# Kernel optimization log

Measured on AMD Instinct MI355X. Metric: run time of the kernel, lower is better.

Reference implementation:

```python
import jax, jax.numpy as jnp
import numpy as np

D_MODEL = 512
N_HEADS = 8
D_K = D_MODEL // N_HEADS


def setup_inputs() -> dict:
    key = jax.random.key(0)
    ks = jax.random.split(key, 11)
    B, L, D = 2, 4096, D_MODEL
    s = 1.0 / np.sqrt(D)
    return {
        "q": jax.random.normal(ks[0], (B, L, D), jnp.float32),
        "k": jax.random.normal(ks[1], (B, L, D), jnp.float32),
        "v": jax.random.normal(ks[2], (B, L, D), jnp.float32),
        "Wq": jax.random.normal(ks[3], (D, D), jnp.float32) * s,
        "bq": jnp.zeros((D,), jnp.float32),
        "Wk": jax.random.normal(ks[4], (D, D), jnp.float32) * s,
        "bk": jnp.zeros((D,), jnp.float32),
        "Wv": jax.random.normal(ks[5], (D, D), jnp.float32) * s,
        "bv": jnp.zeros((D,), jnp.float32),
        "Wo": jax.random.normal(ks[6], (D, D), jnp.float32) * s,
        "bo": jnp.zeros((D,), jnp.float32),
    }


def reference(q, k, v, Wq, bq, Wk, bk, Wv, bv, Wo, bo):
    B, L, D = q.shape
    H, dk = N_HEADS, D_K
    # projections -> [B, H, L, dk]
    qh = (q @ Wq + bq).reshape(B, L, H, dk).transpose(0, 2, 1, 3)
    kh = (k @ Wk + bk).reshape(B, -1, H, dk).transpose(0, 2, 1, 3)
    vh = (v @ Wv + bv).reshape(B, -1, H, dk).transpose(0, 2, 1, 3)
    scores = jnp.einsum("bhqd,bhkd->bhqk", qh, kh) / jnp.sqrt(jnp.float32(dk))
    attn = jax.nn.softmax(scores, axis=-1)  # dropout: eval-mode identity
    ctx = jnp.einsum("bhqk,bhkd->bhqd", attn, vh)
    ctx = ctx.transpose(0, 2, 1, 3).reshape(B, L, D)
    return ctx @ Wo + bo
```

## Files before the change

kernel.cpp:

```cpp
#include <hip/hip_runtime.h>
#include <hip/hip_bf16.h>

#define NB 2
#define NL 4096
#define ND 512
#define NH 8
#define NDK 64
#define NM (NB * NL)
#define QSCALE 0.18033688011112042f

typedef short bf16x8_t __attribute__((ext_vector_type(8)));
typedef float f32x4_t __attribute__((ext_vector_type(4)));

static __device__ __forceinline__ unsigned short f2bs(float f) {
  union { float f; unsigned u; } c; c.f = f;
  unsigned r = c.u + 0x7fffu + ((c.u >> 16) & 1u);
  return (unsigned short)(r >> 16);
}
static __device__ __forceinline__ float bs2f(unsigned short s) {
  union { unsigned u; float f; } c; c.u = ((unsigned)s) << 16; return c.f;
}
static __device__ __forceinline__ unsigned pk_bf16(float a, float b) {
  union { __hip_bfloat162 h; unsigned u; } c;
  c.h = __float22bfloat162_rn(make_float2(a, b));
  return c.u;
}

__global__ __launch_bounds__(256)
void round3_kernel(const float* __restrict__ s0, const float* __restrict__ s1,
                   const float* __restrict__ s2, unsigned short* __restrict__ d0,
                   unsigned short* __restrict__ d1, unsigned short* __restrict__ d2)
{
  const float* s = blockIdx.y == 0 ? s0 : (blockIdx.y == 1 ? s1 : s2);
  unsigned short* d = blockIdx.y == 0 ? d0 : (blockIdx.y == 1 ? d1 : d2);
  const size_t i = ((size_t)blockIdx.x * 256 + threadIdx.x) * 8;
  const float4 f0 = *(const float4*)(s + i);
  const float4 f1 = *(const float4*)(s + i + 4);
  uint4 o;
  o.x = pk_bf16(f0.x, f0.y);
  o.y = pk_bf16(f0.z, f0.w);
  o.z = pk_bf16(f1.x, f1.y);
  o.w = pk_bf16(f1.z, f1.w);
  *(uint4*)(d + i) = o;
}

struct WArgs {
  const float* W[4];
  unsigned short* Th[4];
  unsigned short* Tl[4];
};
__global__ __launch_bounds__(256)
void wsplit_kernel(WArgs a)
{
  const int z = blockIdx.z;
  const float* __restrict__ W = a.W[z];
  const int tid = threadIdx.x;
  const int n = blockIdx.x * 64 + (tid & 63);
  const int kb = blockIdx.y * 64 + (tid >> 6) * 16;
  unsigned short h[16], l[16];
#pragma unroll
  for (int u = 0; u < 16; ++u) {
    const float x = W[(size_t)(kb + u) * ND + n];
    h[u] = f2bs(x);
    l[u] = f2bs(x - bs2f(h[u]));
  }
  unsigned wh[8], wl[8];
#pragma unroll
  for (int p = 0; p < 8; ++p) {
    wh[p] = (unsigned)h[2 * p] | ((unsigned)h[2 * p + 1] << 16);
    wl[p] = (unsigned)l[2 * p] | ((unsigned)l[2 * p + 1] << 16);
  }
  unsigned short* th = a.Th[z] + (size_t)n * ND + kb;
  unsigned short* tl = a.Tl[z] + (size_t)n * ND + kb;
  *(uint4*)th = make_uint4(wh[0], wh[1], wh[2], wh[3]);
  *(uint4*)(th + 8) = make_uint4(wh[4], wh[5], wh[6], wh[7]);
  *(uint4*)tl = make_uint4(wl[0], wl[1], wl[2], wl[3]);
  *(uint4*)(tl + 8) = make_uint4(wl[4], wl[5], wl[6], wl[7]);
}

template <bool ASPLIT, int NJ, int OUTMODE>
__device__ __forceinline__ void gemm_core(
    const unsigned short* __restrict__ Ahi, const unsigned short* __restrict__ Alo,
    const unsigned short* __restrict__ Bh, const unsigned short* __restrict__ Bl,
    const float* __restrict__ bias, unsigned short* __restrict__ outH,
    float* __restrict__ outF, int m0, int n0, float scale)
{
  __shared__ unsigned short AH[128][36];
  __shared__ unsigned short AL[ASPLIT ? 128 : 1][36];
  __shared__ unsigned short BHs[NJ * 16][36];
  __shared__ unsigned short BLs[NJ * 16][36];

  const int tid = threadIdx.x;
  const int lane = tid & 63, w = tid >> 6;
  const int m = lane & 15, quad = lane >> 4;
  const int r = tid >> 1, hf = (tid & 1) * 16;
  const int rb = (NJ == 8) ? (tid >> 1) : (tid >> 2);
  const int cb = (NJ == 8) ? ((tid & 1) * 16) : ((tid & 3) * 8);

  const unsigned short* aRow = Ahi + (size_t)(m0 + r) * ND + hf;
  const unsigned short* alRow = ASPLIT ? (Alo + (size_t)(m0 + r) * ND + hf) : nullptr;
  const unsigned short* bhRow = Bh + (size_t)(n0 + rb) * ND + cb;
  const unsigned short* blRow = Bl + (size_t)(n0 + rb) * ND + cb;

  uint4 ra0 = *(const uint4*)(aRow);
  uint4 ra1 = *(const uint4*)(aRow + 8);
  uint4 rl0, rl1;
  if constexpr (ASPLIT) {
    rl0 = *(const uint4*)(alRow);
    rl1 = *(const uint4*)(alRow + 8);
  }
  uint4 rbh0 = *(const uint4*)(bhRow);
  uint4 rbl0 = *(const uint4*)(blRow);
  uint4 rbh1, rbl1;
  if constexpr (NJ == 8) {
    rbh1 = *(const uint4*)(bhRow + 8);
    rbl1 = *(const uint4*)(blRow + 8);
  }

  f32x4_t acc[2][NJ];
#pragma unroll
  for (int i = 0; i < 2; ++i)
#pragma unroll
    for (int j = 0; j < NJ; ++j) acc[i][j] = (f32x4_t){0.f, 0.f, 0.f, 0.f};

  for (int k0 = 0; k0 < ND; k0 += 32) {
    __syncthreads();
    *(uint4*)&AH[r][hf] = ra0;
    *(uint4*)&AH[r][hf + 8] = ra1;
    if constexpr (ASPLIT) {
      *(uint4*)&AL[r][hf] = rl0;
      *(uint4*)&AL[r][hf + 8] = rl1;
    }
    *(uint4*)&BHs[rb][cb] = rbh0;
    *(uint4*)&BLs[rb][cb] = rbl0;
    if constexpr (NJ == 8) {
      *(uint4*)&BHs[rb][cb + 8] = rbh1;
      *(uint4*)&BLs[rb][cb + 8] = rbl1;
    }
    if (k0 + 32 < ND) {
      const int kn = k0 + 32;
      ra0 = *(const uint4*)(aRow + kn);
      ra1 = *(const uint4*)(aRow + kn + 8);
      if constexpr (ASPLIT) {
        rl0 = *(const uint4*)(alRow + kn);
        rl1 = *(const uint4*)(alRow + kn + 8);
      }
      rbh0 = *(const uint4*)(bhRow + kn);
      rbl0 = *(const uint4*)(blRow + kn);
      if constexpr (NJ == 8) {
        rbh1 = *(const uint4*)(bhRow + kn + 8);
        rbl1 = *(const uint4*)(blRow + kn + 8);
      }
    }
    __syncthreads();

    bf16x8_t ah[2], al[2];
#pragma unroll
    for (int i = 0; i < 2; ++i) {
      ah[i] = *(const bf16x8_t*)&AH[w * 32 + 16 * i + m][quad * 8];
      if constexpr (ASPLIT) al[i] = *(const bf16x8_t*)&AL[w * 32 + 16 * i + m][quad * 8];
    }
#pragma unroll
    for (int j = 0; j < NJ; ++j) {
      const bf16x8_t bhj = *(const bf16x8_t*)&BHs[16 * j + m][quad * 8];
      const bf16x8_t blj = *(const bf16x8_t*)&BLs[16 * j + m][quad * 8];
#pragma unroll
      for (int i = 0; i < 2; ++i) {
        acc[i][j] = __builtin_amdgcn_mfma_f32_16x16x32_bf16(ah[i], bhj, acc[i][j], 0, 0, 0);
        acc[i][j] = __builtin_amdgcn_mfma_f32_16x16x32_bf16(ah[i], blj, acc[i][j], 0, 0, 0);
        if constexpr (ASPLIT)
          acc[i][j] = __builtin_amdgcn_mfma_f32_16x16x32_bf16(al[i], bhj, acc[i][j], 0, 0, 0);
      }
    }
  }

  if constexpr (OUTMODE != 2) {
#pragma unroll
    for (int i = 0; i < 2; ++i)
#pragma unroll
      for (int rr = 0; rr < 4; ++rr) {
        const int mg = m0 + w * 32 + 16 * i + quad * 4 + rr;
#pragma unroll
        for (int j = 0; j < NJ; ++j) {
          const int n = n0 + 16 * j + m;
          const float c = (acc[i][j][rr] + bias[n]) * scale;
          if constexpr (OUTMODE == 0) {
            const int b = mg >> 12, l = mg & (NL - 1);
            const int h = n >> 6, d = n & (NDK - 1);
            outH[(((size_t)(b * NH + h)) * NL + l) * NDK + d] = f2bs(c);
          } else {
            outF[(size_t)mg * ND + n] = c;
          }
        }
      }
  } else {
    unsigned short* T = &BHs[0][0];
    const int bb = m0 >> 12;
    const int lbase = m0 & (NL - 1);
#pragma unroll 1
    for (int p = 0; p < 4; ++p) {
      __syncthreads();
      if (w == p) {
#pragma unroll
        for (int i = 0; i < 2; ++i)
#pragma unroll
          for (int j = 0; j < NJ; ++j) {
            const int n = 16 * j + m;
            const float bv = bias[n0 + n];
            const unsigned w0 = pk_bf16((acc[i][j][0] + bv) * scale,
                                        (acc[i][j][1] + bv) * scale);
            const unsigned w1 = pk_bf16((acc[i][j][2] + bv) * scale,
                                        (acc[i][j][3] + bv) * scale);
            *(uint2*)&T[n * 34 + 16 * i + quad * 4] = make_uint2(w0, w1);
          }
      }
      __syncthreads();
      const int n = tid >> 1;
      const int l0 = (tid & 1) * 16;
      const uint4 t0 = *(const uint4*)&T[n * 34 + l0];
      const uint4 t1 = *(const uint4*)&T[n * 34 + l0 + 8];
      const int ng = n0 + n;
      const int h = ng >> 6, d = ng & (NDK - 1);
      unsigned short* dp =
          outH + (((size_t)(bb * NH + h)) * NDK + d) * NL + lbase + 32 * p + l0;
      *(uint4*)dp = t0;
      *(uint4*)(dp + 8) = t1;
    }
  }
}

struct ProjArgs {
  const unsigned short* A[3];
  const unsigned short* Bh[3];
  const unsigned short* Bl[3];
  const float* bias[3];
  unsigned short* out[3];
  float scale[3];
};
__global__ __launch_bounds__(256, 3)
void gemm_proj_kernel(ProjArgs a)
{
  const int z = blockIdx.z;
  if (z < 2)
    gemm_core<false, 8, 0>(a.A[z], nullptr, a.Bh[z], a.Bl[z], a.bias[z], a.out[z],
                           nullptr, blockIdx.x * 128, blockIdx.y * 128, a.scale[z]);
  else
    gemm_core<false, 8, 2>(a.A[2], nullptr, a.Bh[2], a.Bl[2], a.bias[2], a.out[2],
                           nullptr, blockIdx.x * 128, blockIdx.y * 128, a.scale[2]);
}
__global__ __launch_bounds__(256, 3)
void gemm_out_kernel(const unsigned short* __restrict__ Ahi,
                     const unsigned short* __restrict__ Alo,
                     const unsigned short* __restrict__ Bh,
                     const unsigned short* __restrict__ Bl,
                     const float* __restrict__ bias, float* __restrict__ out)
{
  gemm_core<true, 4, 1>(Ahi, Alo, Bh, Bl, bias, nullptr, out,
                        blockIdx.x * 128, blockIdx.y * 64, 1.0f);
}

__global__ __launch_bounds__(256, 4)
void attn_kernel(const unsigned short* __restrict__ qh, const unsigned short* __restrict__ kh,
                 const unsigned short* __restrict__ vt_g, float* __restrict__ op,
                 float* __restrict__ lp)
{
  __shared__ unsigned short Ks[64][72];
  __shared__ unsigned short Vt[64][72];
  __shared__ unsigned Pt[64][67];

  const int tid = threadIdx.x;
  const int w = tid >> 6;
  const int lane = tid & 63;
  const int m = lane & 15;
  const int quad = lane >> 4;

  const int bid = blockIdx.x;
  const int half = bid & 1;
  const int qt = (bid >> 1) & 31;
  const int bh = bid >> 6;
  const int kt0 = half * 32, kt1 = kt0 + 32;
  const unsigned short* qb = qh + (size_t)bh * NL * NDK;
  const unsigned short* kb = kh + (size_t)bh * NL * NDK;
  const unsigned short* vb = vt_g + (size_t)bh * NDK * NL;

  bf16x8_t aq[2][2];
#pragma unroll
  for (int mt = 0; mt < 2; ++mt) {
    const unsigned short* qsrc =
        qb + (size_t)(qt * 128 + w * 32 + mt * 16 + m) * NDK + quad * 8;
    aq[mt][0] = *(const bf16x8_t*)(qsrc);
    aq[mt][1] = *(const bf16x8_t*)(qsrc + 32);
  }

  const short ob = (short)0x3F80;
  const bf16x8_t ones = {ob, ob, ob, ob, ob, ob, ob, ob};

  f32x4_t o[2][4];
#pragma unroll
  for (int mt = 0; mt < 2; ++mt)
#pragma unroll
    for (int nt = 0; nt < 4; ++nt) o[mt][nt] = (f32x4_t){0.f, 0.f, 0.f, 0.f};
  f32x4_t ol[2];
  ol[0] = (f32x4_t){0.f, 0.f, 0.f, 0.f};
  ol[1] = (f32x4_t){0.f, 0.f, 0.f, 0.f};

  const int kr = tid >> 2;
  const int kc = (tid & 3) * 16;

  uint4 pk0, pk1, pv0, pv1;
  {
    const unsigned short* ksrc = kb + (size_t)(kt0 * 64 + kr) * NDK + kc;
    pk0 = *(const uint4*)ksrc;
    pk1 = *(const uint4*)(ksrc + 8);
    const unsigned short* vsrc = vb + (size_t)kr * NL + kt0 * 64 + kc;
    pv0 = *(const uint4*)vsrc;
    pv1 = *(const uint4*)(vsrc + 8);
  }

  for (int kt = kt0; kt < kt1; ++kt) {
    __syncthreads();
    *(uint4*)&Ks[kr][kc] = pk0;
    *(uint4*)&Ks[kr][kc + 8] = pk1;
    *(uint4*)&Vt[kr][kc] = pv0;
    *(uint4*)&Vt[kr][kc + 8] = pv1;
    if (kt + 1 < kt1) {
      const unsigned short* ksrc = kb + (size_t)((kt + 1) * 64 + kr) * NDK + kc;
      pk0 = *(const uint4*)ksrc;
      pk1 = *(const uint4*)(ksrc + 8);
      const unsigned short* vsrc = vb + (size_t)kr * NL + (kt + 1) * 64 + kc;
      pv0 = *(const uint4*)vsrc;
      pv1 = *(const uint4*)(vsrc + 8);
    }
    __syncthreads();

#pragma unroll
    for (int nt = 0; nt < 4; ++nt) {
      const bf16x8_t b0 = *(const bf16x8_t*)&Ks[16 * nt + m][quad * 8];
      const bf16x8_t b1 = *(const bf16x8_t*)&Ks[16 * nt + m][quad * 8 + 32];
      f32x4_t s0 = (f32x4_t){0.f, 0.f, 0.f, 0.f};
      s0 = __builtin_amdgcn_mfma_f32_16x16x32_bf16(aq[0][0], b0, s0, 0, 0, 0);
      s0 = __builtin_amdgcn_mfma_f32_16x16x32_bf16(aq[0][1], b1, s0, 0, 0, 0);
      f32x4_t s1 = (f32x4_t){0.f, 0.f, 0.f, 0.f};
      s1 = __builtin_amdgcn_mfma_f32_16x16x32_bf16(aq[1][0], b0, s1, 0, 0, 0);
      s1 = __builtin_amdgcn_mfma_f32_16x16x32_bf16(aq[1][1], b1, s1, 0, 0, 0);
      unsigned pw[4];
#pragma unroll
      for (int r = 0; r < 4; ++r)
        pw[r] = pk_bf16(exp2f(s0[r]), exp2f(s1[r]));
      *(uint4*)&Pt[16 * nt + m][w * 16 + quad * 4] =
          make_uint4(pw[0], pw[1], pw[2], pw[3]);
    }

#pragma unroll
    for (int kb2 = 0; kb2 < 2; ++kb2) {
      unsigned pwv[8];
#pragma unroll
      for (int j = 0; j < 8; ++j)
        pwv[j] = Pt[kb2 * 32 + quad * 8 + j][w * 16 + m];
      union { bf16x8_t v; unsigned d[4]; } pa0, pa1;
#pragma unroll
      for (int t = 0; t < 4; ++t) {
        pa0.d[t] = (pwv[2 * t] & 0xffffu) | (pwv[2 * t + 1] << 16);
        pa1.d[t] = (pwv[2 * t] >> 16) | (pwv[2 * t + 1] & 0xffff0000u);
      }
#pragma unroll
      for (int nt = 0; nt < 4; ++nt) {
        const bf16x8_t vb0 = *(const bf16x8_t*)&Vt[16 * nt + m][kb2 * 32 + quad * 8];
        o[0][nt] = __builtin_amdgcn_mfma_f32_16x16x32_bf16(pa0.v, vb0, o[0][nt], 0, 0, 0);
        o[1][nt] = __builtin_amdgcn_mfma_f32_16x16x32_bf16(pa1.v, vb0, o[1][nt], 0, 0, 0);
      }
      ol[0] = __builtin_amdgcn_mfma_f32_16x16x32_bf16(pa0.v, ones, ol[0], 0, 0, 0);
      ol[1] = __builtin_amdgcn_mfma_f32_16x16x32_bf16(pa1.v, ones, ol[1], 0, 0, 0);
    }
  }

  const size_t pbase = (size_t)(half * 16 + bh) * NL;
#pragma unroll
  for (int mt = 0; mt < 2; ++mt) {
    const int q0 = qt * 128 + w * 32 + mt * 16 + quad * 4;
    if (m == 0)
      *(float4*)&lp[pbase + q0] =
          make_float4(ol[mt][0], ol[mt][1], ol[mt][2], ol[mt][3]);
#pragma unroll
    for (int r = 0; r < 4; ++r) {
      float* dst = op + (pbase + q0 + r) * NDK;
#pragma unroll
      for (int nt = 0; nt < 4; ++nt) dst[16 * nt + m] = o[mt][nt][r];
    }
  }
}

__global__ __launch_bounds__(256)
void merge_kernel(const float* __restrict__ op, const float* __restrict__ lp,
                  unsigned short* __restrict__ ctxh, unsigned short* __restrict__ ctxl)
{
  const size_t t = (size_t)blockIdx.x * 256 + threadIdx.x;
  const int d0 = (int)(t & 7) * 8;
  const size_t row = t >> 3;
  const float l0 = lp[row];
  const float l1 = lp[row + (size_t)16 * NL];
  const float inv = 1.0f / (l0 + l1);
  const float* a = op + row * NDK + d0;
  const float* c = a + (size_t)16 * NL * NDK;
  const float4 a0 = *(const float4*)a, a1 = *(const float4*)(a + 4);
  const float4 c0 = *(const float4*)c, c1 = *(const float4*)(c + 4);
  const float x[8] = {(a0.x + c0.x) * inv, (a0.y + c0.y) * inv,
                      (a0.z + c0.z) * inv, (a0.w + c0.w) * inv,
                      (a1.x + c1.x) * inv, (a1.y + c1.y) * inv,
                      (a1.z + c1.z) * inv, (a1.w + c1.w) * inv};
  unsigned short hs[8], ls[8];
#pragma unroll
  for (int u = 0; u < 8; ++u) {
    hs[u] = f2bs(x[u]);
    ls[u] = f2bs(x[u] - bs2f(hs[u]));
  }
  const int bh = (int)(row >> 12), l = (int)(row & (NL - 1));
  const int b = bh >> 3, h = bh & 7;
  const size_t dst = ((size_t)(b * NL + l)) * ND + h * 64 + d0;
  uint4 uh, ul;
  uh.x = (unsigned)hs[0] | ((unsigned)hs[1] << 16);
  uh.y = (unsigned)hs[2] | ((unsigned)hs[3] << 16);
  uh.z = (unsigned)hs[4] | ((unsigned)hs[5] << 16);
  uh.w = (unsigned)hs[6] | ((unsigned)hs[7] << 16);
  ul.x = (unsigned)ls[0] | ((unsigned)ls[1] << 16);
  ul.y = (unsigned)ls[2] | ((unsigned)ls[3] << 16);
  ul.z = (unsigned)ls[4] | ((unsigned)ls[5] << 16);
  ul.w = (unsigned)ls[6] | ((unsigned)ls[7] << 16);
  *(uint4*)(ctxh + dst) = uh;
  *(uint4*)(ctxl + dst) = ul;
}

extern "C" void kernel_launch(void* const* d_in, const int* in_sizes, int n_in,
                              void* d_out, int out_size, void* d_ws, size_t ws_size,
                              hipStream_t stream)
{
  const float* q  = (const float*)d_in[0];
  const float* k  = (const float*)d_in[1];
  const float* v  = (const float*)d_in[2];
  const float* Wq = (const float*)d_in[3];
  const float* bq = (const float*)d_in[4];
  const float* Wk = (const float*)d_in[5];
  const float* bk = (const float*)d_in[6];
  const float* Wv = (const float*)d_in[7];
  const float* bv = (const float*)d_in[8];
  const float* Wo = (const float*)d_in[9];
  const float* bo = (const float*)d_in[10];

  const size_t PLANE = (size_t)NM * ND;
  unsigned short* wt = (unsigned short*)d_ws;
  unsigned short* qhp = wt + 8 * (size_t)ND * ND;
  unsigned short* khp = qhp + PLANE;
  unsigned short* vtp = khp + PLANE;
  float* op = (float*)(vtp + PLANE);
  float* lp = op + 2 * (size_t)16 * NL * NDK;
  unsigned short* qb = (unsigned short*)op;
  unsigned short* kb = qb + PLANE;
  unsigned short* vb = kb + PLANE;
  unsigned short* ctxh = qhp;
  unsigned short* ctxl = khp;

  unsigned short* wth[4], *wtl[4];
  for (int i = 0; i < 4; ++i) {
    wth[i] = wt + (size_t)(2 * i) * ND * ND;
    wtl[i] = wt + (size_t)(2 * i + 1) * ND * ND;
  }

  round3_kernel<<<dim3(PLANE / (256 * 8), 3), 256, 0, stream>>>(q, k, v, qb, kb, vb);

  WArgs wa;
  wa.W[0] = Wq; wa.W[1] = Wk; wa.W[2] = Wv; wa.W[3] = Wo;
  for (int i = 0; i < 4; ++i) { wa.Th[i] = wth[i]; wa.Tl[i] = wtl[i]; }
  wsplit_kernel<<<dim3(8, 8, 4), 256, 0, stream>>>(wa);

  ProjArgs pa;
  pa.A[0] = qb; pa.A[1] = kb; pa.A[2] = vb;
  pa.Bh[0] = wth[0]; pa.Bl[0] = wtl[0];
  pa.Bh[1] = wth[1]; pa.Bl[1] = wtl[1];
  pa.Bh[2] = wth[2]; pa.Bl[2] = wtl[2];
  pa.bias[0] = bq; pa.bias[1] = bk; pa.bias[2] = bv;
  pa.out[0] = qhp; pa.out[1] = khp; pa.out[2] = vtp;
  pa.scale[0] = QSCALE; pa.scale[1] = 1.0f; pa.scale[2] = 1.0f;
  gemm_proj_kernel<<<dim3(NM / 128, ND / 128, 3), 256, 0, stream>>>(pa);

  attn_kernel<<<dim3(NB * NH * (NL / 128) * 2), 256, 0, stream>>>(qhp, khp, vtp, op, lp);

  merge_kernel<<<dim3((16 * NL * NDK) / (256 * 8)), 256, 0, stream>>>(op, lp, ctxh, ctxl);

  gemm_out_kernel<<<dim3(NM / 128, ND / 64), 256, 0, stream>>>(
      ctxh, ctxl, wth[3], wtl[3], bo, (float*)d_out);
}
```

Baseline: 289.4 us.

## Keep P in registers via transposed QK^T, swizzle LDS, enlarge query tile

Computes S^T = K·Q^T so the MFMA output layout lines up directly with the A-operand layout for the P·V product, so the Pt shared-memory round trip and its repacking are gone. K and V tiles are stored in LDS with an XOR swizzle instead of padding. Each wave now handles 64 query rows (256 per block), which doubles reuse of every K/V tile loaded and halves the grid. In exchange, register pressure rises (launch bounds drop to 2 blocks per CU) and there are fewer blocks in flight.

```diff
diff --git a/kernel.cpp b/kernel.cpp
--- a/kernel.cpp
+++ b/kernel.cpp
@@ -259,35 +259,35 @@
                         blockIdx.x * 128, blockIdx.y * 64, 1.0f);
 }
 
-__global__ __launch_bounds__(256, 4)
+__global__ __launch_bounds__(256, 2)
 void attn_kernel(const unsigned short* __restrict__ qh, const unsigned short* __restrict__ kh,
                  const unsigned short* __restrict__ vt_g, float* __restrict__ op,
                  float* __restrict__ lp)
 {
-  __shared__ unsigned short Ks[64][72];
-  __shared__ unsigned short Vt[64][72];
-  __shared__ unsigned Pt[64][67];
+  __shared__ unsigned short Ks[64 * 64];
+  __shared__ unsigned short Vt[64 * 64];
 
   const int tid = threadIdx.x;
   const int w = tid >> 6;
   const int lane = tid & 63;
   const int m = lane & 15;
   const int quad = lane >> 4;
+  const int sw = m & 7;
 
   const int bid = blockIdx.x;
   const int half = bid & 1;
-  const int qt = (bid >> 1) & 31;
-  const int bh = bid >> 6;
+  const int qt = (bid >> 1) & 15;
+  const int bh = bid >> 5;
   const int kt0 = half * 32, kt1 = kt0 + 32;
   const unsigned short* qb = qh + (size_t)bh * NL * NDK;
   const unsigned short* kb = kh + (size_t)bh * NL * NDK;
   const unsigned short* vb = vt_g + (size_t)bh * NDK * NL;
 
-  bf16x8_t aq[2][2];
-#pragma unroll
-  for (int mt = 0; mt < 2; ++mt) {
+  bf16x8_t aq[4][2];
+#pragma unroll
+  for (int mt = 0; mt < 4; ++mt) {
     const unsigned short* qsrc =
-        qb + (size_t)(qt * 128 + w * 32 + mt * 16 + m) * NDK + quad * 8;
+        qb + (size_t)(qt * 256 + w * 64 + mt * 16 + m) * NDK + quad * 8;
     aq[mt][0] = *(const bf16x8_t*)(qsrc);
     aq[mt][1] = *(const bf16x8_t*)(qsrc + 32);
   }
@@ -295,17 +295,26 @@
   const short ob = (short)0x3F80;
   const bf16x8_t ones = {ob, ob, ob, ob, ob, ob, ob, ob};
 
-  f32x4_t o[2][4];
-#pragma unroll
-  for (int mt = 0; mt < 2; ++mt)
+  f32x4_t o[4][4];
+#pragma unroll
+  for (int mt = 0; mt < 4; ++mt)
 #pragma unroll
     for (int nt = 0; nt < 4; ++nt) o[mt][nt] = (f32x4_t){0.f, 0.f, 0.f, 0.f};
-  f32x4_t ol[2];
-  ol[0] = (f32x4_t){0.f, 0.f, 0.f, 0.f};
-  ol[1] = (f32x4_t){0.f, 0.f, 0.f, 0.f};
+  f32x4_t ol[4];
+#pragma unroll
+  for (int mt = 0; mt < 4; ++mt) ol[mt] = (f32x4_t){0.f, 0.f, 0.f, 0.f};
 
   const int kr = tid >> 2;
-  const int kc = (tid & 3) * 16;
+  const int kcb = tid & 3;
+  const int kc = kcb * 16;
+  const int r7 = kr & 7;
+  const int st0 = kr * 64 + ((2 * kcb) ^ r7) * 8;
+  const int st1 = kr * 64 + ((2 * kcb + 1) ^ r7) * 8;
+
+  const int rowb = m * 64;
+  const int ck0 = rowb + ((quad ^ sw) * 8);
+  const int ck1 = rowb + (((quad + 4) ^ sw) * 8);
+  const int vq = quad >> 1, vo = (quad & 1) * 4;
 
   uint4 pk0, pk1, pv0, pv1;
   {
@@ -319,10 +328,10 @@
 
   for (int kt = kt0; kt < kt1; ++kt) {
     __syncthreads();
-    *(uint4*)&Ks[kr][kc] = pk0;
-    *(uint4*)&Ks[kr][kc + 8] = pk1;
-    *(uint4*)&Vt[kr][kc] = pv0;
-    *(uint4*)&Vt[kr][kc + 8] = pv1;
+    *(uint4*)&Ks[st0] = pk0;
+    *(uint4*)&Ks[st1] = pk1;
+    *(uint4*)&Vt[st0] = pv0;
+    *(uint4*)&Vt[st1] = pv1;
     if (kt + 1 < kt1) {
       const unsigned short* ksrc = kb + (size_t)((kt + 1) * 64 + kr) * NDK + kc;
       pk0 = *(const uint4*)ksrc;
@@ -334,50 +343,51 @@
     __syncthreads();
 
 #pragma unroll
-    for (int nt = 0; nt < 4; ++nt) {
-      const bf16x8_t b0 = *(const bf16x8_t*)&Ks[16 * nt + m][quad * 8];
-      const bf16x8_t b1 = *(const bf16x8_t*)&Ks[16 * nt + m][quad * 8 + 32];
-      f32x4_t s0 = (f32x4_t){0.f, 0.f, 0.f, 0.f};
-      s0 = __builtin_amdgcn_mfma_f32_16x16x32_bf16(aq[0][0], b0, s0, 0, 0, 0);
-      s0 = __builtin_amdgcn_mfma_f32_16x16x32_bf16(aq[0][1], b1, s0, 0, 0, 0);
-      f32x4_t s1 = (f32x4_t){0.f, 0.f, 0.f, 0.f};
-      s1 = __builtin_amdgcn_mfma_f32_16x16x32_bf16(aq[1][0], b0, s1, 0, 0, 0);
-      s1 = __builtin_amdgcn_mfma_f32_16x16x32_bf16(aq[1][1], b1, s1, 0, 0, 0);
-      unsigned pw[4];
-#pragma unroll
-      for (int r = 0; r < 4; ++r)
-        pw[r] = pk_bf16(exp2f(s0[r]), exp2f(s1[r]));
-      *(uint4*)&Pt[16 * nt + m][w * 16 + quad * 4] =
-          make_uint4(pw[0], pw[1], pw[2], pw[3]);
-    }
-
-#pragma unroll
-    for (int kb2 = 0; kb2 < 2; ++kb2) {
-      unsigned pwv[8];
-#pragma unroll
-      for (int j = 0; j < 8; ++j)
-        pwv[j] = Pt[kb2 * 32 + quad * 8 + j][w * 16 + m];
-      union { bf16x8_t v; unsigned d[4]; } pa0, pa1;
-#pragma unroll
-      for (int t = 0; t < 4; ++t) {
-        pa0.d[t] = (pwv[2 * t] & 0xffffu) | (pwv[2 * t + 1] << 16);
-        pa1.d[t] = (pwv[2 * t] >> 16) | (pwv[2 * t + 1] & 0xffff0000u);
+    for (int c = 0; c < 2; ++c) {
+      unsigned paw[4][4];
+#pragma unroll
+      for (int t = 0; t < 2; ++t) {
+        const int nt = 2 * c + t;
+        const bf16x8_t kf0 = *(const bf16x8_t*)&Ks[nt * 1024 + ck0];
+        const bf16x8_t kf1 = *(const bf16x8_t*)&Ks[nt * 1024 + ck1];
+#pragma unroll
+        for (int mt = 0; mt < 4; ++mt) {
+          f32x4_t s = (f32x4_t){0.f, 0.f, 0.f, 0.f};
+          s = __builtin_amdgcn_mfma_f32_16x16x32_bf16(kf0, aq[mt][0], s, 0, 0, 0);
+          s = __builtin_amdgcn_mfma_f32_16x16x32_bf16(kf1, aq[mt][1], s, 0, 0, 0);
+          paw[mt][2 * t]     = pk_bf16(exp2f(s[0]), exp2f(s[1]));
+          paw[mt][2 * t + 1] = pk_bf16(exp2f(s[2]), exp2f(s[3]));
+        }
+      }
+      union U { bf16x8_t v; unsigned d[4]; };
+      U pa[4];
+#pragma unroll
+      for (int mt = 0; mt < 4; ++mt) {
+        pa[mt].d[0] = paw[mt][0];
+        pa[mt].d[1] = paw[mt][1];
+        pa[mt].d[2] = paw[mt][2];
+        pa[mt].d[3] = paw[mt][3];
       }
 #pragma unroll
       for (int nt = 0; nt < 4; ++nt) {
-        const bf16x8_t vb0 = *(const bf16x8_t*)&Vt[16 * nt + m][kb2 * 32 + quad * 8];
-        o[0][nt] = __builtin_amdgcn_mfma_f32_16x16x32_bf16(pa0.v, vb0, o[0][nt], 0, 0, 0);
-        o[1][nt] = __builtin_amdgcn_mfma_f32_16x16x32_bf16(pa1.v, vb0, o[1][nt], 0, 0, 0);
-      }
-      ol[0] = __builtin_amdgcn_mfma_f32_16x16x32_bf16(pa0.v, ones, ol[0], 0, 0, 0);
-      ol[1] = __builtin_amdgcn_mfma_f32_16x16x32_bf16(pa1.v, ones, ol[1], 0, 0, 0);
+        union { bf16x8_t v; uint2 h[2]; } vf;
+        const int vrow = nt * 1024 + rowb;
+        vf.h[0] = *(const uint2*)&Vt[vrow + ((4 * c + vq) ^ sw) * 8 + vo];
+        vf.h[1] = *(const uint2*)&Vt[vrow + ((4 * c + 2 + vq) ^ sw) * 8 + vo];
+#pragma unroll
+        for (int mt = 0; mt < 4; ++mt)
+          o[mt][nt] = __builtin_amdgcn_mfma_f32_16x16x32_bf16(pa[mt].v, vf.v, o[mt][nt], 0, 0, 0);
+      }
+#pragma unroll
+      for (int mt = 0; mt < 4; ++mt)
+        ol[mt] = __builtin_amdgcn_mfma_f32_16x16x32_bf16(pa[mt].v, ones, ol[mt], 0, 0, 0);
     }
   }
 
   const size_t pbase = (size_t)(half * 16 + bh) * NL;
 #pragma unroll
-  for (int mt = 0; mt < 2; ++mt) {
-    const int q0 = qt * 128 + w * 32 + mt * 16 + quad * 4;
+  for (int mt = 0; mt < 4; ++mt) {
+    const int q0 = qt * 256 + w * 64 + mt * 16 + quad * 4;
     if (m == 0)
       *(float4*)&lp[pbase + q0] =
           make_float4(ol[mt][0], ol[mt][1], ol[mt][2], ol[mt][3]);
@@ -482,7 +492,7 @@
   pa.scale[0] = QSCALE; pa.scale[1] = 1.0f; pa.scale[2] = 1.0f;
   gemm_proj_kernel<<<dim3(NM / 128, ND / 128, 3), 256, 0, stream>>>(pa);
 
-  attn_kernel<<<dim3(NB * NH * (NL / 128) * 2), 256, 0, stream>>>(qhp, khp, vtp, op, lp);
+  attn_kernel<<<dim3(NB * NH * (NL / 256) * 2), 256, 0, stream>>>(qhp, khp, vtp, op, lp);
 
   merge_kernel<<<dim3((16 * NL * NDK) / (256 * 8)), 256, 0, stream>>>(op, lp, ctxh, ctxl);
 
```

After: 279.5 us. 1.04x faster.
